# Kernel optimization log

Measured on AMD Instinct MI355X. Metric: run time of the kernel, lower is better.

The kernel has to match this reference:

```python
import jax, jax.numpy as jnp
import numpy as np
import math

C_S, C_Z = 384, 128
N_HEAD, C = 12, 16
N_QP, N_PV = 4, 8
B, N_RES = 1, 384


def quat_to_rot(q):
    # q: (..., 4) unnormalized quaternion -> (..., 3, 3) rotation matrix
    q = q / jnp.linalg.norm(q, axis=-1, keepdims=True)
    w, x, y, z = q[..., 0], q[..., 1], q[..., 2], q[..., 3]
    R = jnp.stack([
        1 - 2 * (y * y + z * z), 2 * (x * y - w * z), 2 * (x * z + w * y),
        2 * (x * y + w * z), 1 - 2 * (x * x + z * z), 2 * (y * z - w * x),
        2 * (x * z - w * y), 2 * (y * z + w * x), 1 - 2 * (x * x + y * y),
    ], axis=-1)
    return R.reshape(q.shape[:-1] + (3, 3))


def warp_3d_point(T, p):
    # T: (..., 1, 1, N, 4, 4) rigid transforms; p: (..., H, P, N, 3)
    R = T[..., :3, :3]
    t = T[..., :3, 3]
    return jnp.squeeze(R @ p[..., None], -1) + t


def warp_3d_point_inv(T, p):
    # Inverse rigid transform: R^T (p - t)
    R = T[..., :3, :3]
    t = T[..., :3, 3]
    return jnp.squeeze(jnp.swapaxes(R, -1, -2) @ (p - t)[..., None], -1)


def setup_inputs() -> dict:
    key = jax.random.key(0)
    ks = jax.random.split(key, 24)
    s = jax.random.normal(ks[0], (B, N_RES, C_S), dtype=jnp.float32)
    z = jax.random.normal(ks[1], (B, N_RES, N_RES, C_Z), dtype=jnp.float32)
    # Build rigid backbone transforms T (rotation from random quaternion + translation)
    quat = jax.random.normal(ks[2], (B, N_RES, 4), dtype=jnp.float32)
    trans = jax.random.normal(ks[3], (B, N_RES, 3), dtype=jnp.float32) * 10.0
    R = quat_to_rot(quat)
    T = jnp.zeros((B, N_RES, 4, 4), dtype=jnp.float32)
    T = T.at[..., :3, :3].set(R)
    T = T.at[..., :3, 3].set(trans)
    T = T.at[..., 3, 3].set(1.0)

    def lin(k, din, dout):
        kw, kb = jax.random.split(k)
        W = jax.random.normal(kw, (din, dout), dtype=jnp.float32) * 0.02
        b = jax.random.normal(kb, (dout,), dtype=jnp.float32) * 0.01
        return W, b

    Wq, bq = lin(ks[4], C_S, N_HEAD * C)
    Wk, bk = lin(ks[5], C_S, N_HEAD * C)
    Wv, bv = lin(ks[6], C_S, N_HEAD * C)
    Wqp, bqp = lin(ks[7], C_S, 3 * N_QP * N_HEAD)
    Wkp, bkp = lin(ks[8], C_S, 3 * N_QP * N_HEAD)
    Wvp, bvp = lin(ks[9], C_S, 3 * N_PV * N_HEAD)
    Wb, bb = lin(ks[10], C_Z, N_HEAD)
    d_out_in = N_HEAD * C_Z + N_HEAD * C + N_HEAD * 4 * N_PV
    Wo, bo = lin(ks[11], d_out_in, C_S)
    head_weights = jax.random.normal(ks[12], (N_HEAD,), dtype=jnp.float32) * 0.1
    return dict(s=s, z=z, T=T, Wq=Wq, bq=bq, Wk=Wk, bk=bk, Wv=Wv, bv=bv,
                Wqp=Wqp, bqp=bqp, Wkp=Wkp, bkp=bkp, Wvp=Wvp, bvp=bvp,
                Wb=Wb, bb=bb, Wo=Wo, bo=bo, head_weights=head_weights)


def ipa_forward(s, z, T, Wq, bq, Wk, bk, Wv, bv, Wqp, bqp, Wkp, bkp,
                Wvp, bvp, Wb, bb, Wo, bo, head_weights):
    batch = s.shape[:-2]
    n = s.shape[-2]
    # --- prepare qkv ---
    def heads(x):  # (..., N, H*C) -> (..., H, N, C)
        return jnp.moveaxis(x.reshape(batch + (n, N_HEAD, C)), -3, -2)
    q = heads(s @ Wq + bq)
    k = heads(s @ Wk + bk)
    v = heads(s @ Wv + bv)

    def pts(x, P):  # (..., N, 3*H*P) -> (..., H, P, N, 3)
        x = x.reshape(batch + (n, 3, N_HEAD, P))
        return jnp.moveaxis(x, (-4, -3), (-2, -1))
    qp = pts(s @ Wqp + bqp, N_QP)
    kp = pts(s @ Wkp + bkp, N_QP)
    vp = pts(s @ Wvp + bvp, N_PV)

    # --- attention scores (Alg 22 line 7) ---
    wc = math.sqrt(2.0 / (9.0 * N_QP))
    wl = math.sqrt(1.0 / 3.0)
    gamma = jax.nn.softplus(head_weights).reshape(-1, 1, 1)  # (H,1,1)
    q = q * (1.0 / math.sqrt(C))
    bias = jnp.moveaxis(z @ Wb + bb, -1, -3)  # (..., H, N, N)
    qk = jnp.einsum('...hic,...hjc->...hij', q, k)
    T_bc = T.reshape(batch + (1, 1, n, 4, 4))
    tqp = warp_3d_point(T_bc, qp)[..., :, None, :]   # (..., H, QP, N, 1, 3)
    tkp = warp_3d_point(T_bc, kp)[..., None, :, :]   # (..., H, QP, 1, N, 3)
    sq_dist = jnp.sum((tqp - tkp) ** 2, axis=-1)      # (..., H, QP, N, N)
    qpkp_term = gamma * (wc / 2.0) * jnp.sum(sq_dist, axis=-3)  # (..., H, N, N)
    att = jax.nn.softmax(wl * (qk + bias - qpkp_term), axis=-1)

    # --- outputs ---
    pairwise = jnp.einsum('...ijc,...hij->...hic', z, att)
    pairwise = jnp.moveaxis(pairwise, -3, -2).reshape(batch + (n, N_HEAD * C_Z))
    v_out = jnp.einsum('...hij,...hjc->...hic', att, v)
    v_out = jnp.moveaxis(v_out, -3, -2).reshape(batch + (n, N_HEAD * C))
    vt = warp_3d_point(T_bc, vp)                                # (..., H, PV, N, 3)
    v_att = jnp.einsum('...hij,...hkjp->...hkip', att, vt)     # (..., H, PV, N, 3)
    v_tr = warp_3d_point_inv(T_bc, v_att)                       # (..., H, PV, N, 3)
    v_tr = jnp.einsum('...hpic->...ichp', v_tr)                 # (..., N, 3, H, PV)
    norm = jnp.linalg.norm(v_tr, axis=-3, keepdims=True)        # (..., N, 1, H, PV)
    vp_norm = norm.reshape(batch + (n, N_HEAD * N_PV))
    vp_out = v_tr.reshape(batch + (n, 3 * N_HEAD * N_PV))

    out = jnp.concatenate([v_out, vp_out, vp_norm, pairwise], axis=-1)
    return out @ Wo + bo


def reference(s, z, T, Wq, bq, Wk, bk, Wv, bv, Wqp, bqp, Wkp, bkp,
              Wvp, bvp, Wb, bb, Wo, bo, head_weights):
    return ipa_forward(s, z, T, Wq, bq, Wk, bk, Wv, bv, Wqp, bqp, Wkp, bkp,
                       Wvp, bvp, Wb, bb, Wo, bo, head_weights)
```

## Files before the change

kernel.cpp:

```cpp
#include <hip/hip_runtime.h>
#include <math.h>

#define NRES 384
#define NH   12
#define WLc 0.5773502691896258f
#define WCc 0.23570226039551587f

typedef __attribute__((ext_vector_type(8))) short short8;
typedef __attribute__((ext_vector_type(4))) float f32x4;

#define OFF_P    0
#define OFF_BIASB 0
#define OFF_QE   884736
#define OFF_KE   1032192
#define OFF_VET  1179648
#define OFF_O40  1290240
#define OFF_SBF  1474560
#define OFF_WCT  1548288
#define OFF_BCT  1769472
#define OFF_WOT  1770624
#define OFF_CAT  2176128
#define OFF_ATT  2581632

__device__ inline unsigned short f2bf(float f) {
    union { float f; unsigned u; } v; v.f = f;
    unsigned u = v.u;
    return (unsigned short)((u + 0x7FFFu + ((u >> 16) & 1u)) >> 16);
}
__device__ inline float bf2f(unsigned short h) {
    union { unsigned u; float f; } v; v.u = ((unsigned)h) << 16;
    return v.f;
}

__global__ __launch_bounds__(256) void pack_kernel(
    const float* __restrict__ s,
    const float* __restrict__ Wq,  const float* __restrict__ bq,
    const float* __restrict__ Wk,  const float* __restrict__ bk,
    const float* __restrict__ Wv,  const float* __restrict__ bv,
    const float* __restrict__ Wqp, const float* __restrict__ bqp,
    const float* __restrict__ Wkp, const float* __restrict__ bkp,
    const float* __restrict__ Wvp, const float* __restrict__ bvp,
    const float* __restrict__ Wo,
    float* __restrict__ ws)
{
    int id = blockIdx.x * 256 + threadIdx.x;
    unsigned short* sbf  = (unsigned short*)(ws + OFF_SBF);
    unsigned short* wct  = (unsigned short*)(ws + OFF_WCT);
    unsigned short* wot  = (unsigned short*)(ws + OFF_WOT);
    float* bct = ws + OFF_BCT;

    if (id < 36864) {
        const float4 v = ((const float4*)s)[id];
        unsigned short r[4] = { f2bf(v.x), f2bf(v.y), f2bf(v.z), f2bf(v.w) };
        *(uint2*)(sbf + id * 4) = *(uint2*)r;
        return;
    }
    id -= 36864;
    if (id < 55296) {
        int n = id / 48, k8 = (id % 48) * 8;
        const float* W; int dout, col;
        if      (n < 192) { W = Wq;  dout = 192; col = n; }
        else if (n < 384) { W = Wk;  dout = 192; col = n - 192; }
        else if (n < 576) { W = Wv;  dout = 192; col = n - 384; }
        else if (n < 720) { W = Wqp; dout = 144; col = n - 576; }
        else if (n < 864) { W = Wkp; dout = 144; col = n - 720; }
        else              { W = Wvp; dout = 288; col = n - 864; }
        unsigned short r[8];
        #pragma unroll
        for (int j = 0; j < 8; j++) r[j] = f2bf(W[(size_t)(k8 + j) * dout + col]);
        *(uint4*)(wct + (size_t)n * 384 + k8) = *(uint4*)r;
        return;
    }
    id -= 55296;
    if (id < 101376) {
        int n = id / 264, k8 = (id % 264) * 8;
        unsigned short r[8];
        #pragma unroll
        for (int j = 0; j < 8; j++) r[j] = f2bf(Wo[(size_t)(k8 + j) * 384 + n]);
        *(uint4*)(wot + (size_t)n * 2112 + k8) = *(uint4*)r;
        return;
    }
    id -= 101376;
    if (id < 1152) {
        int n = id; float b;
        if      (n < 192) b = bq[n];
        else if (n < 384) b = bk[n - 192];
        else if (n < 576) b = bv[n - 384];
        else if (n < 720) b = bqp[n - 576];
        else if (n < 864) b = bkp[n - 720];
        else              b = bvp[n - 864];
        bct[n] = b;
    }
}

__global__ __launch_bounds__(256) void proj_mfma(float* __restrict__ ws)
{
    const unsigned short* sbf = (const unsigned short*)(ws + OFF_SBF);
    const unsigned short* wct = (const unsigned short*)(ws + OFF_WCT);
    const float* bct = ws + OFF_BCT;
    float* P = ws + OFF_P;

    int t = threadIdx.x, w = t >> 6, lane = t & 63;
    int m = lane & 15, q = lane >> 4;
    int n0 = blockIdx.x * 64, m0 = blockIdx.y * 64 + w * 16;

    f32x4 acc[4] = {0};
    const unsigned short* arow = sbf + (size_t)(m0 + m) * 384;
    #pragma unroll 4
    for (int s = 0; s < 12; s++) {
        int k = s * 32 + q * 8;
        short8 a = *(const short8*)(arow + k);
        #pragma unroll
        for (int nt = 0; nt < 4; nt++) {
            short8 b = *(const short8*)(wct + (size_t)(n0 + nt * 16 + m) * 384 + k);
            acc[nt] = __builtin_amdgcn_mfma_f32_16x16x32_bf16(a, b, acc[nt], 0, 0, 0);
        }
    }
    #pragma unroll
    for (int nt = 0; nt < 4; nt++) {
        int col = n0 + nt * 16 + m;
        float bias = bct[col];
        #pragma unroll
        for (int r = 0; r < 4; r++) {
            int row = m0 + q * 4 + r;
            P[(size_t)row * 1152 + col] = acc[nt][r] + bias;
        }
    }
}

__global__ __launch_bounds__(256) void prep_kernel(
    const float* __restrict__ T, const float* __restrict__ hw,
    float* __restrict__ ws)
{
    int id = blockIdx.x * 256 + threadIdx.x;
    if (id >= NH * NRES) return;
    int h = id / NRES, i = id % NRES;
    const float* P = ws + OFF_P;
    const float* pr = P + (size_t)i * 1152;

    float R[3][3], tr[3];
    #pragma unroll
    for (int r = 0; r < 3; r++) {
        #pragma unroll
        for (int c = 0; c < 3; c++) R[r][c] = T[i * 16 + r * 4 + c];
        tr[r] = T[i * 16 + r * 4 + 3];
    }
    float x = hw[h];
    float g = (x > 20.f) ? x : log1pf(expf(x));

    float* Qe = ws + OFF_QE + (size_t)(h * NRES + i) * 32;
    float* Ke = ws + OFF_KE + (size_t)(h * NRES + i) * 32;
    #pragma unroll
    for (int c = 0; c < 16; c++) {
        Qe[c] = WLc * 0.25f * pr[h * 16 + c];
        Ke[c] = pr[192 + h * 16 + c];
    }
    float sqq = 0.f, sqk = 0.f;
    float gw = WLc * g * WCc;
    #pragma unroll
    for (int p = 0; p < 4; p++) {
        float a0 = pr[576 + 0 * 48 + h * 4 + p];
        float a1 = pr[576 + 1 * 48 + h * 4 + p];
        float a2 = pr[576 + 2 * 48 + h * 4 + p];
        float b0 = pr[720 + 0 * 48 + h * 4 + p];
        float b1 = pr[720 + 1 * 48 + h * 4 + p];
        float b2 = pr[720 + 2 * 48 + h * 4 + p];
        #pragma unroll
        for (int r = 0; r < 3; r++) {
            float tq = R[r][0] * a0 + R[r][1] * a1 + R[r][2] * a2 + tr[r];
            float tk = R[r][0] * b0 + R[r][1] * b1 + R[r][2] * b2 + tr[r];
            Qe[16 + p * 3 + r] = gw * tq;
            Ke[16 + p * 3 + r] = tk;
            sqq += tq * tq;  sqk += tk * tk;
        }
    }
    Qe[28] = -0.5f * gw;  Qe[29] = -0.5f * gw * sqq;  Qe[30] = 0.f; Qe[31] = 0.f;
    Ke[28] = sqk;         Ke[29] = 1.f;               Ke[30] = 0.f; Ke[31] = 0.f;

    unsigned short* vet = (unsigned short*)(ws + OFF_VET);
    #pragma unroll
    for (int c = 0; c < 16; c++)
        vet[(size_t)(h * 48 + c) * 384 + i] = f2bf(pr[384 + h * 16 + c]);
    #pragma unroll
    for (int p = 0; p < 8; p++) {
        float a0 = pr[864 + 0 * 96 + h * 8 + p];
        float a1 = pr[864 + 1 * 96 + h * 8 + p];
        float a2 = pr[864 + 2 * 96 + h * 8 + p];
        #pragma unroll
        for (int r = 0; r < 3; r++)
            vet[(size_t)(h * 48 + 16 + p * 3 + r) * 384 + i] =
                f2bf(R[r][0] * a0 + R[r][1] * a1 + R[r][2] * a2 + tr[r]);
    }
    #pragma unroll
    for (int c = 40; c < 48; c++) vet[(size_t)(h * 48 + c) * 384 + i] = 0;
}

__global__ __launch_bounds__(256) void bias_mfma(
    const float* __restrict__ z, const float* __restrict__ Wb,
    const float* __restrict__ bb, float* __restrict__ ws)
{
    __shared__ unsigned short zb[64 * 136];
    __shared__ unsigned short wbT[16 * 136];
    __shared__ float sbb[16];
    unsigned short* biasb = (unsigned short*)(ws + OFF_BIASB);

    int t = threadIdx.x;
    size_t m0 = (size_t)blockIdx.x * 64;

    {
        int r = t >> 2, co = (t & 3) * 32;
        const float* zr = z + (m0 + r) * 128 + co;
        #pragma unroll
        for (int u = 0; u < 4; u++) {
            float4 v0 = ((const float4*)zr)[u * 2 + 0];
            float4 v1 = ((const float4*)zr)[u * 2 + 1];
            unsigned short rr[8] = { f2bf(v0.x), f2bf(v0.y), f2bf(v0.z), f2bf(v0.w),
                                     f2bf(v1.x), f2bf(v1.y), f2bf(v1.z), f2bf(v1.w) };
            *(uint4*)(zb + r * 136 + co + u * 8) = *(uint4*)rr;
        }
    }
    if (t < 128) {
        #pragma unroll
        for (int h = 0; h < 12; h++) wbT[h * 136 + t] = f2bf(Wb[t * 12 + h]);
        #pragma unroll
        for (int h = 12; h < 16; h++) wbT[h * 136 + t] = 0;
    }
    if (t < 16) sbb[t] = (t < 12) ? bb[t] : 0.f;
    __syncthreads();

    int w = t >> 6, lane = t & 63;
    int m = lane & 15, q = lane >> 4;
    f32x4 acc = {0};
    #pragma unroll
    for (int s = 0; s < 4; s++) {
        int k = s * 32 + q * 8;
        short8 a = *(const short8*)(zb + (w * 16 + m) * 136 + k);
        short8 b = *(const short8*)(wbT + m * 136 + k);
        acc = __builtin_amdgcn_mfma_f32_16x16x32_bf16(a, b, acc, 0, 0, 0);
    }
    int h = m;
    if (h < 12) {
        #pragma unroll
        for (int r = 0; r < 4; r++) {
            size_t ri = m0 + w * 16 + q * 4 + r;
            biasb[(size_t)h * 147456 + ri] = f2bf(WLc * (acc[r] + sbb[h]));
        }
    }
}

__global__ __launch_bounds__(512) void logits_kernel(float* __restrict__ ws)
{
    __shared__ float sQe[8 * 32];
    __shared__ float sLg[8][384];
    __shared__ float sMS[16];

    int h = blockIdx.y, i0 = blockIdx.x * 8;
    int t = threadIdx.x;
    const float* Qe = ws + OFF_QE;
    const float* Ke = ws + OFF_KE;
    const unsigned short* biasb = (const unsigned short*)(ws + OFF_BIASB);
    unsigned short* attb = (unsigned short*)(ws + OFF_ATT);

    if (t < 256)
        sQe[t] = Qe[(size_t)(h * 384 + i0 + (t >> 5)) * 32 + (t & 31)];
    __syncthreads();

    float lgv[8];
    if (t < 384) {
        int j = t;
        float ke[32];
        const float4* kr = (const float4*)(Ke + (size_t)(h * 384 + j) * 32);
        #pragma unroll
        for (int u = 0; u < 8; u++) { float4 v = kr[u]; ke[u*4]=v.x; ke[u*4+1]=v.y; ke[u*4+2]=v.z; ke[u*4+3]=v.w; }
        #pragma unroll
        for (int ii = 0; ii < 8; ii++) {
            float acc = 0.f;
            #pragma unroll
            for (int c = 0; c < 32; c++) acc += sQe[ii * 32 + c] * ke[c];
            acc += bf2f(biasb[(size_t)(h * 384 + i0 + ii) * 384 + j]);
            lgv[ii] = acc;
            sLg[ii][j] = acc;
        }
    }
    __syncthreads();
    {
        int w = t >> 6, lane = t & 63;
        float vv[6], mx = -1e30f;
        #pragma unroll
        for (int u = 0; u < 6; u++) { vv[u] = sLg[w][lane + 64 * u]; mx = fmaxf(mx, vv[u]); }
        #pragma unroll
        for (int off = 1; off < 64; off <<= 1) mx = fmaxf(mx, __shfl_xor(mx, off));
        float sm = 0.f;
        #pragma unroll
        for (int u = 0; u < 6; u++) sm += __expf(vv[u] - mx);
        #pragma unroll
        for (int off = 1; off < 64; off <<= 1) sm += __shfl_xor(sm, off);
        if (lane == 0) { sMS[w] = mx; sMS[8 + w] = sm; }
    }
    __syncthreads();
    if (t < 384) {
        int j = t;
        #pragma unroll
        for (int ii = 0; ii < 8; ii++) {
            float a = __expf(lgv[ii] - sMS[ii]) * (1.0f / sMS[8 + ii]);
            attb[(size_t)(h * 384 + i0 + ii) * 384 + j] = f2bf(a);
        }
    }
}

__global__ __launch_bounds__(128) void out40_mfma(float* __restrict__ ws)
{
    const unsigned short* attb = (const unsigned short*)(ws + OFF_ATT);
    const unsigned short* vet  = (const unsigned short*)(ws + OFF_VET);
    float* o40 = ws + OFF_O40;

    int h = blockIdx.y;
    int t = threadIdx.x, w = t >> 6, lane = t & 63;
    int m = lane & 15, q = lane >> 4;
    int m0 = blockIdx.x * 32 + w * 16;

    f32x4 acc[3] = {0};
    const unsigned short* arow = attb + (size_t)(h * 384 + m0 + m) * 384;
    #pragma unroll 3
    for (int s = 0; s < 12; s++) {
        int k = s * 32 + q * 8;
        short8 a = *(const short8*)(arow + k);
        #pragma unroll
        for (int nt = 0; nt < 3; nt++) {
            short8 b = *(const short8*)(vet + (size_t)(h * 48 + nt * 16 + m) * 384 + k);
            acc[nt] = __builtin_amdgcn_mfma_f32_16x16x32_bf16(a, b, acc[nt], 0, 0, 0);
        }
    }
    #pragma unroll
    for (int nt = 0; nt < 3; nt++) {
        int c = nt * 16 + m;
        if (c < 40) {
            #pragma unroll
            for (int r = 0; r < 4; r++) {
                int row = m0 + q * 4 + r;
                o40[(size_t)row * 480 + h * 40 + c] = acc[nt][r];
            }
        }
    }
}

__global__ __launch_bounds__(256) void pairwise_pts(
    const float* __restrict__ z, const float* __restrict__ T,
    float* __restrict__ ws)
{
    __shared__ unsigned short zt[128 * 40];
    __shared__ float sT16[16];

    int i = blockIdx.x;
    int t = threadIdx.x, w = t >> 6, lane = t & 63;
    int m = lane & 15, q = lane >> 4;
    const unsigned short* attb = (const unsigned short*)(ws + OFF_ATT);
    unsigned short* catb = (unsigned short*)(ws + OFF_CAT) ;
    const float* o40 = ws + OFF_O40;

    if (t < 16) sT16[t] = T[i * 16 + t];

    f32x4 acc0 = {0}, acc1 = {0};
    int cst = t & 63, jg = t >> 6;
    for (int kt = 0; kt < 12; kt++) {
        int j0 = kt * 32;
        __syncthreads();
        {
            int j8 = j0 + jg * 8;
            const float* zb = z + ((size_t)i * 384 + j8) * 128 + cst;
            unsigned short r0[8], r1[8];
            #pragma unroll
            for (int jj = 0; jj < 8; jj++) {
                r0[jj] = f2bf(zb[(size_t)jj * 128]);
                r1[jj] = f2bf(zb[(size_t)jj * 128 + 64]);
            }
            *(uint4*)(zt + cst * 40 + jg * 8)        = *(uint4*)r0;
            *(uint4*)(zt + (cst + 64) * 40 + jg * 8) = *(uint4*)r1;
        }
        __syncthreads();
        short8 a;
        if (m < 12) a = *(const short8*)(attb + ((size_t)(m * 384 + i)) * 384 + j0 + q * 8);
        else        a = (short8){0,0,0,0,0,0,0,0};
        short8 b0 = *(const short8*)(zt + (w * 32 + m) * 40 + q * 8);
        short8 b1 = *(const short8*)(zt + (w * 32 + 16 + m) * 40 + q * 8);
        acc0 = __builtin_amdgcn_mfma_f32_16x16x32_bf16(a, b0, acc0, 0, 0, 0);
        acc1 = __builtin_amdgcn_mfma_f32_16x16x32_bf16(a, b1, acc1, 0, 0, 0);
    }
    {
        unsigned short* crow = catb + (size_t)i * 2112 + 576;
        #pragma unroll
        for (int r = 0; r < 4; r++) {
            int h = q * 4 + r;
            if (h < 12) {
                crow[h * 128 + w * 32 + m]      = f2bf(acc0[r]);
                crow[h * 128 + w * 32 + 16 + m] = f2bf(acc1[r]);
            }
        }
    }
    __syncthreads();
    if (t < 192)
        catb[(size_t)i * 2112 + t] = f2bf(o40[(size_t)i * 480 + (t >> 4) * 40 + (t & 15)]);
    if (t < 96) {
        int h = t >> 3, p = t & 7;
        const float* o = o40 + (size_t)i * 480 + h * 40 + 16 + p * 3;
        float x0 = o[0] - sT16[3];
        float x1 = o[1] - sT16[7];
        float x2 = o[2] - sT16[11];
        float r0 = sT16[0] * x0 + sT16[4] * x1 + sT16[8]  * x2;
        float r1 = sT16[1] * x0 + sT16[5] * x1 + sT16[9]  * x2;
        float r2 = sT16[2] * x0 + sT16[6] * x1 + sT16[10] * x2;
        unsigned short* crow = catb + (size_t)i * 2112;
        crow[192 + 0 * 96 + h * 8 + p] = f2bf(r0);
        crow[192 + 1 * 96 + h * 8 + p] = f2bf(r1);
        crow[192 + 2 * 96 + h * 8 + p] = f2bf(r2);
        crow[480 + h * 8 + p] = f2bf(sqrtf(r0 * r0 + r1 * r1 + r2 * r2));
    }
}

__global__ __launch_bounds__(256) void out_init(const float* __restrict__ bo, float* __restrict__ out)
{
    int idx = blockIdx.x * 256 + threadIdx.x;
    if (idx < 384 * 384) out[idx] = bo[idx % 384];
}

__global__ __launch_bounds__(256) void outgemm_mfma(float* __restrict__ ws, float* __restrict__ out)
{
    const unsigned short* catb = (const unsigned short*)(ws + OFF_CAT);
    const unsigned short* wot  = (const unsigned short*)(ws + OFF_WOT);

    int t = threadIdx.x, w = t >> 6, lane = t & 63;
    int m = lane & 15, q = lane >> 4;
    int n0 = blockIdx.x * 64, m0 = blockIdx.y * 64 + w * 16;
    int kbase = blockIdx.z * 704;

    f32x4 acc[4] = {0};
    const unsigned short* arow = catb + (size_t)(m0 + m) * 2112;
    #pragma unroll 2
    for (int s = 0; s < 22; s++) {
        int k = kbase + s * 32 + q * 8;
        short8 a = *(const short8*)(arow + k);
        #pragma unroll
        for (int nt = 0; nt < 4; nt++) {
            short8 b = *(const short8*)(wot + (size_t)(n0 + nt * 16 + m) * 2112 + k);
            acc[nt] = __builtin_amdgcn_mfma_f32_16x16x32_bf16(a, b, acc[nt], 0, 0, 0);
        }
    }
    #pragma unroll
    for (int nt = 0; nt < 4; nt++) {
        int col = n0 + nt * 16 + m;
        #pragma unroll
        for (int r = 0; r < 4; r++) {
            int row = m0 + q * 4 + r;
            atomicAdd(&out[(size_t)row * 384 + col], acc[nt][r]);
        }
    }
}

extern "C" void kernel_launch(void* const* d_in, const int* in_sizes, int n_in,
                              void* d_out, int out_size, void* d_ws, size_t ws_size,
                              hipStream_t stream)
{
    const float* s   = (const float*)d_in[0];
    const float* z   = (const float*)d_in[1];
    const float* T   = (const float*)d_in[2];
    const float* Wq  = (const float*)d_in[3];
    const float* bq  = (const float*)d_in[4];
    const float* Wk  = (const float*)d_in[5];
    const float* bk  = (const float*)d_in[6];
    const float* Wv  = (const float*)d_in[7];
    const float* bv  = (const float*)d_in[8];
    const float* Wqp = (const float*)d_in[9];
    const float* bqp = (const float*)d_in[10];
    const float* Wkp = (const float*)d_in[11];
    const float* bkp = (const float*)d_in[12];
    const float* Wvp = (const float*)d_in[13];
    const float* bvp = (const float*)d_in[14];
    const float* Wb  = (const float*)d_in[15];
    const float* bb  = (const float*)d_in[16];
    const float* Wo  = (const float*)d_in[17];
    const float* bo  = (const float*)d_in[18];
    const float* hw  = (const float*)d_in[19];
    float* ws  = (float*)d_ws;
    float* out = (float*)d_out;

    pack_kernel<<<(36864 + 55296 + 101376 + 1152 + 255) / 256, 256, 0, stream>>>(
        s, Wq, bq, Wk, bk, Wv, bv, Wqp, bqp, Wkp, bkp, Wvp, bvp, Wo, ws);
    proj_mfma<<<dim3(18, 6), 256, 0, stream>>>(ws);
    prep_kernel<<<18, 256, 0, stream>>>(T, hw, ws);
    bias_mfma<<<2304, 256, 0, stream>>>(z, Wb, bb, ws);
    logits_kernel<<<dim3(48, 12), 512, 0, stream>>>(ws);
    out40_mfma<<<dim3(12, 12), 128, 0, stream>>>(ws);
    pairwise_pts<<<384, 256, 0, stream>>>(z, T, ws);
    out_init<<<576, 256, 0, stream>>>(bo, out);
    outgemm_mfma<<<dim3(6, 6, 3), 256, 0, stream>>>(ws, out);
}
```

Baseline: 241.0 us.

## Fuse pair bias, softmax and attention outputs into one flash-style kernel

Replaces the separate bias, logits, softmax, value-output and pairwise kernels with a single per-residue flash kernel. It reads z once per row chunk, computes the pair bias, runs an online softmax, and accumulates value, point and pairwise outputs without writing the full bias and attention matrices to memory. The code also switches from bf16 to fp16 MFMA and parallelises prep across residues. In exchange, only 384 blocks do serial chunk loops and the online rescaling adds some work.

```diff
diff --git a/kernel.cpp b/kernel.cpp
--- a/kernel.cpp
+++ b/kernel.cpp
@@ -6,31 +6,19 @@
 #define WLc 0.5773502691896258f
 #define WCc 0.23570226039551587f
 
-typedef __attribute__((ext_vector_type(8))) short short8;
+typedef __attribute__((ext_vector_type(8))) _Float16 half8;
 typedef __attribute__((ext_vector_type(4))) float f32x4;
 
 #define OFF_P    0
-#define OFF_BIASB 0
-#define OFF_QE   884736
-#define OFF_KE   1032192
-#define OFF_VET  1179648
-#define OFF_O40  1290240
-#define OFF_SBF  1474560
-#define OFF_WCT  1548288
-#define OFF_BCT  1769472
-#define OFF_WOT  1770624
-#define OFF_CAT  2176128
-#define OFF_ATT  2581632
-
-__device__ inline unsigned short f2bf(float f) {
-    union { float f; unsigned u; } v; v.f = f;
-    unsigned u = v.u;
-    return (unsigned short)((u + 0x7FFFu + ((u >> 16) & 1u)) >> 16);
-}
-__device__ inline float bf2f(unsigned short h) {
-    union { unsigned u; float f; } v; v.u = ((unsigned)h) << 16;
-    return v.f;
-}
+#define OFF_QE   442368
+#define OFF_KE   589824
+#define OFF_VET  737280
+#define OFF_SH   847872
+#define OFF_WCT  921600
+#define OFF_BCT  1142784
+#define OFF_WOT  1143936
+#define OFF_WBT  1549440
+#define OFF_CAT  1550464
 
 __global__ __launch_bounds__(256) void pack_kernel(
     const float* __restrict__ s,
@@ -40,19 +28,20 @@
     const float* __restrict__ Wqp, const float* __restrict__ bqp,
     const float* __restrict__ Wkp, const float* __restrict__ bkp,
     const float* __restrict__ Wvp, const float* __restrict__ bvp,
-    const float* __restrict__ Wo,
+    const float* __restrict__ Wb,  const float* __restrict__ Wo,
     float* __restrict__ ws)
 {
     int id = blockIdx.x * 256 + threadIdx.x;
-    unsigned short* sbf  = (unsigned short*)(ws + OFF_SBF);
-    unsigned short* wct  = (unsigned short*)(ws + OFF_WCT);
-    unsigned short* wot  = (unsigned short*)(ws + OFF_WOT);
+    _Float16* sh  = (_Float16*)(ws + OFF_SH);
+    _Float16* wct = (_Float16*)(ws + OFF_WCT);
+    _Float16* wot = (_Float16*)(ws + OFF_WOT);
+    _Float16* wbt = (_Float16*)(ws + OFF_WBT);
     float* bct = ws + OFF_BCT;
 
     if (id < 36864) {
         const float4 v = ((const float4*)s)[id];
-        unsigned short r[4] = { f2bf(v.x), f2bf(v.y), f2bf(v.z), f2bf(v.w) };
-        *(uint2*)(sbf + id * 4) = *(uint2*)r;
+        _Float16 r[4] = { (_Float16)v.x, (_Float16)v.y, (_Float16)v.z, (_Float16)v.w };
+        *(uint2*)(sh + id * 4) = *(uint2*)r;
         return;
     }
     id -= 36864;
@@ -65,22 +54,28 @@
         else if (n < 720) { W = Wqp; dout = 144; col = n - 576; }
         else if (n < 864) { W = Wkp; dout = 144; col = n - 720; }
         else              { W = Wvp; dout = 288; col = n - 864; }
-        unsigned short r[8];
-        #pragma unroll
-        for (int j = 0; j < 8; j++) r[j] = f2bf(W[(size_t)(k8 + j) * dout + col]);
-        *(uint4*)(wct + (size_t)n * 384 + k8) = *(uint4*)r;
+        half8 r;
+        #pragma unroll
+        for (int j = 0; j < 8; j++) r[j] = (_Float16)W[(size_t)(k8 + j) * dout + col];
+        *(half8*)(wct + (size_t)n * 384 + k8) = r;
         return;
     }
     id -= 55296;
     if (id < 101376) {
         int n = id / 264, k8 = (id % 264) * 8;
-        unsigned short r[8];
-        #pragma unroll
-        for (int j = 0; j < 8; j++) r[j] = f2bf(Wo[(size_t)(k8 + j) * 384 + n]);
-        *(uint4*)(wot + (size_t)n * 2112 + k8) = *(uint4*)r;
+        half8 r;
+        #pragma unroll
+        for (int j = 0; j < 8; j++) r[j] = (_Float16)Wo[(size_t)(k8 + j) * 384 + n];
+        *(half8*)(wot + (size_t)n * 2112 + k8) = r;
         return;
     }
     id -= 101376;
+    if (id < 2048) {
+        int h = id >> 7, c = id & 127;
+        wbt[h * 128 + c] = (h < 12) ? (_Float16)(WLc * Wb[c * 12 + h]) : (_Float16)0.f;
+        return;
+    }
+    id -= 2048;
     if (id < 1152) {
         int n = id; float b;
         if      (n < 192) b = bq[n];
@@ -95,8 +90,8 @@
 
 __global__ __launch_bounds__(256) void proj_mfma(float* __restrict__ ws)
 {
-    const unsigned short* sbf = (const unsigned short*)(ws + OFF_SBF);
-    const unsigned short* wct = (const unsigned short*)(ws + OFF_WCT);
+    const _Float16* sh  = (const _Float16*)(ws + OFF_SH);
+    const _Float16* wct = (const _Float16*)(ws + OFF_WCT);
     const float* bct = ws + OFF_BCT;
     float* P = ws + OFF_P;
 
@@ -105,15 +100,15 @@
     int n0 = blockIdx.x * 64, m0 = blockIdx.y * 64 + w * 16;
 
     f32x4 acc[4] = {0};
-    const unsigned short* arow = sbf + (size_t)(m0 + m) * 384;
+    const _Float16* arow = sh + (size_t)(m0 + m) * 384;
     #pragma unroll 4
     for (int s = 0; s < 12; s++) {
         int k = s * 32 + q * 8;
-        short8 a = *(const short8*)(arow + k);
+        half8 a = *(const half8*)(arow + k);
         #pragma unroll
         for (int nt = 0; nt < 4; nt++) {
-            short8 b = *(const short8*)(wct + (size_t)(n0 + nt * 16 + m) * 384 + k);
-            acc[nt] = __builtin_amdgcn_mfma_f32_16x16x32_bf16(a, b, acc[nt], 0, 0, 0);
+            half8 b = *(const half8*)(wct + (size_t)(n0 + nt * 16 + m) * 384 + k);
+            acc[nt] = __builtin_amdgcn_mfma_f32_16x16x32_f16(a, b, acc[nt], 0, 0, 0);
         }
     }
     #pragma unroll
@@ -121,299 +116,256 @@
         int col = n0 + nt * 16 + m;
         float bias = bct[col];
         #pragma unroll
-        for (int r = 0; r < 4; r++) {
-            int row = m0 + q * 4 + r;
-            P[(size_t)row * 1152 + col] = acc[nt][r] + bias;
-        }
-    }
-}
-
-__global__ __launch_bounds__(256) void prep_kernel(
+        for (int r = 0; r < 4; r++)
+            P[(size_t)(m0 + q * 4 + r) * 1152 + col] = acc[nt][r] + bias;
+    }
+}
+
+__global__ __launch_bounds__(192) void prep_kernel(
     const float* __restrict__ T, const float* __restrict__ hw,
     float* __restrict__ ws)
 {
-    int id = blockIdx.x * 256 + threadIdx.x;
-    if (id >= NH * NRES) return;
-    int h = id / NRES, i = id % NRES;
-    const float* P = ws + OFF_P;
-    const float* pr = P + (size_t)i * 1152;
-
-    float R[3][3], tr[3];
-    #pragma unroll
-    for (int r = 0; r < 3; r++) {
-        #pragma unroll
-        for (int c = 0; c < 3; c++) R[r][c] = T[i * 16 + r * 4 + c];
-        tr[r] = T[i * 16 + r * 4 + 3];
-    }
-    float x = hw[h];
-    float g = (x > 20.f) ? x : log1pf(expf(x));
-
-    float* Qe = ws + OFF_QE + (size_t)(h * NRES + i) * 32;
-    float* Ke = ws + OFF_KE + (size_t)(h * NRES + i) * 32;
-    #pragma unroll
-    for (int c = 0; c < 16; c++) {
-        Qe[c] = WLc * 0.25f * pr[h * 16 + c];
-        Ke[c] = pr[192 + h * 16 + c];
-    }
-    float sqq = 0.f, sqk = 0.f;
-    float gw = WLc * g * WCc;
-    #pragma unroll
-    for (int p = 0; p < 4; p++) {
-        float a0 = pr[576 + 0 * 48 + h * 4 + p];
-        float a1 = pr[576 + 1 * 48 + h * 4 + p];
-        float a2 = pr[576 + 2 * 48 + h * 4 + p];
-        float b0 = pr[720 + 0 * 48 + h * 4 + p];
-        float b1 = pr[720 + 1 * 48 + h * 4 + p];
-        float b2 = pr[720 + 2 * 48 + h * 4 + p];
-        #pragma unroll
-        for (int r = 0; r < 3; r++) {
-            float tq = R[r][0] * a0 + R[r][1] * a1 + R[r][2] * a2 + tr[r];
-            float tk = R[r][0] * b0 + R[r][1] * b1 + R[r][2] * b2 + tr[r];
-            Qe[16 + p * 3 + r] = gw * tq;
-            Ke[16 + p * 3 + r] = tk;
-            sqq += tq * tq;  sqk += tk * tk;
-        }
-    }
-    Qe[28] = -0.5f * gw;  Qe[29] = -0.5f * gw * sqq;  Qe[30] = 0.f; Qe[31] = 0.f;
-    Ke[28] = sqk;         Ke[29] = 1.f;               Ke[30] = 0.f; Ke[31] = 0.f;
-
-    unsigned short* vet = (unsigned short*)(ws + OFF_VET);
-    #pragma unroll
-    for (int c = 0; c < 16; c++)
-        vet[(size_t)(h * 48 + c) * 384 + i] = f2bf(pr[384 + h * 16 + c]);
-    #pragma unroll
-    for (int p = 0; p < 8; p++) {
-        float a0 = pr[864 + 0 * 96 + h * 8 + p];
-        float a1 = pr[864 + 1 * 96 + h * 8 + p];
-        float a2 = pr[864 + 2 * 96 + h * 8 + p];
-        #pragma unroll
-        for (int r = 0; r < 3; r++)
-            vet[(size_t)(h * 48 + 16 + p * 3 + r) * 384 + i] =
-                f2bf(R[r][0] * a0 + R[r][1] * a1 + R[r][2] * a2 + tr[r]);
-    }
-    #pragma unroll
-    for (int c = 40; c < 48; c++) vet[(size_t)(h * 48 + c) * 384 + i] = 0;
-}
-
-__global__ __launch_bounds__(256) void bias_mfma(
-    const float* __restrict__ z, const float* __restrict__ Wb,
+    int i = blockIdx.x, t = threadIdx.x;
+    const float* pr = ws + OFF_P + (size_t)i * 1152;
+    float* Qe = ws + OFF_QE;
+    float* Ke = ws + OFF_KE;
+    _Float16* vet = (_Float16*)(ws + OFF_VET);
+
+    __shared__ float sT[16], sG[12];
+    __shared__ float sTQ[12][4][3], sTK[12][4][3];
+    if (t < 16) sT[t] = T[i * 16 + t];
+    if (t < 12) { float x = hw[t]; sG[t] = (x > 20.f) ? x : log1pf(__expf(x)); }
+    __syncthreads();
+    float R00=sT[0],R01=sT[1],R02=sT[2],t0=sT[3];
+    float R10=sT[4],R11=sT[5],R12=sT[6],t1=sT[7];
+    float R20=sT[8],R21=sT[9],R22=sT[10],t2=sT[11];
+
+    if (t < 48) {
+        int h = t >> 2, p = t & 3;
+        float a0 = pr[576 + 0*48 + h*4 + p], a1 = pr[576 + 1*48 + h*4 + p], a2 = pr[576 + 2*48 + h*4 + p];
+        sTQ[h][p][0] = R00*a0 + R01*a1 + R02*a2 + t0;
+        sTQ[h][p][1] = R10*a0 + R11*a1 + R12*a2 + t1;
+        sTQ[h][p][2] = R20*a0 + R21*a1 + R22*a2 + t2;
+    } else if (t < 96) {
+        int tt = t - 48, h = tt >> 2, p = tt & 3;
+        float a0 = pr[720 + 0*48 + h*4 + p], a1 = pr[720 + 1*48 + h*4 + p], a2 = pr[720 + 2*48 + h*4 + p];
+        sTK[h][p][0] = R00*a0 + R01*a1 + R02*a2 + t0;
+        sTK[h][p][1] = R10*a0 + R11*a1 + R12*a2 + t1;
+        sTK[h][p][2] = R20*a0 + R21*a1 + R22*a2 + t2;
+    } else {
+        int tt = t - 96, h = tt >> 3, p = tt & 7;
+        float a0 = pr[864 + 0*96 + h*8 + p], a1 = pr[864 + 1*96 + h*8 + p], a2 = pr[864 + 2*96 + h*8 + p];
+        vet[(size_t)(h*48 + 16 + p*3 + 0) * 384 + i] = (_Float16)(R00*a0 + R01*a1 + R02*a2 + t0);
+        vet[(size_t)(h*48 + 16 + p*3 + 1) * 384 + i] = (_Float16)(R10*a0 + R11*a1 + R12*a2 + t1);
+        vet[(size_t)(h*48 + 16 + p*3 + 2) * 384 + i] = (_Float16)(R20*a0 + R21*a1 + R22*a2 + t2);
+    }
+    {
+        int h = t >> 4, c = t & 15;
+        vet[(size_t)(h*48 + c) * 384 + i] = (_Float16)pr[384 + h*16 + c];
+        if (t < 96) vet[(size_t)((t>>3)*48 + 40 + (t&7)) * 384 + i] = (_Float16)0.f;
+    }
+    {
+        int h = t >> 4, c = t & 15;
+        Qe[(size_t)i*384 + h*32 + c] = WLc * 0.25f * pr[h*16 + c];
+        Ke[((size_t)h*384 + i)*32 + c] = pr[192 + h*16 + c];
+    }
+    __syncthreads();
+    if (t < 144) {
+        int h = t / 12, d = t % 12, p = d / 3, r = d % 3;
+        float gw = WLc * sG[h] * WCc;
+        Qe[(size_t)i*384 + h*32 + 16 + d] = gw * sTQ[h][p][r];
+        Ke[((size_t)h*384 + i)*32 + 16 + d] = sTK[h][p][r];
+    }
+    if (t < 12) {
+        int h = t;
+        float sqq = 0.f, sqk = 0.f;
+        #pragma unroll
+        for (int p = 0; p < 4; p++)
+            #pragma unroll
+            for (int r = 0; r < 3; r++) { sqq += sTQ[h][p][r]*sTQ[h][p][r]; sqk += sTK[h][p][r]*sTK[h][p][r]; }
+        float gw = WLc * sG[h] * WCc;
+        Qe[(size_t)i*384 + h*32 + 28] = -0.5f * gw;
+        Qe[(size_t)i*384 + h*32 + 29] = -0.5f * gw * sqq;
+        Qe[(size_t)i*384 + h*32 + 30] = 0.f;
+        Qe[(size_t)i*384 + h*32 + 31] = 0.f;
+        Ke[((size_t)h*384 + i)*32 + 28] = sqk;
+        Ke[((size_t)h*384 + i)*32 + 29] = 1.f;
+        Ke[((size_t)h*384 + i)*32 + 30] = 0.f;
+        Ke[((size_t)h*384 + i)*32 + 31] = 0.f;
+    }
+}
+
+__global__ __launch_bounds__(256) void flash_kernel(
+    const float* __restrict__ z, const float* __restrict__ T,
     const float* __restrict__ bb, float* __restrict__ ws)
 {
-    __shared__ unsigned short zb[64 * 136];
-    __shared__ unsigned short wbT[16 * 136];
-    __shared__ float sbb[16];
-    unsigned short* biasb = (unsigned short*)(ws + OFF_BIASB);
-
-    int t = threadIdx.x;
-    size_t m0 = (size_t)blockIdx.x * 64;
-
-    {
-        int r = t >> 2, co = (t & 3) * 32;
-        const float* zr = z + (m0 + r) * 128 + co;
-        #pragma unroll
-        for (int u = 0; u < 4; u++) {
-            float4 v0 = ((const float4*)zr)[u * 2 + 0];
-            float4 v1 = ((const float4*)zr)[u * 2 + 1];
-            unsigned short rr[8] = { f2bf(v0.x), f2bf(v0.y), f2bf(v0.z), f2bf(v0.w),
-                                     f2bf(v1.x), f2bf(v1.y), f2bf(v1.z), f2bf(v1.w) };
-            *(uint4*)(zb + r * 136 + co + u * 8) = *(uint4*)rr;
-        }
-    }
-    if (t < 128) {
-        #pragma unroll
-        for (int h = 0; h < 12; h++) wbT[h * 136 + t] = f2bf(Wb[t * 12 + h]);
-        #pragma unroll
-        for (int h = 12; h < 16; h++) wbT[h * 136 + t] = 0;
-    }
-    if (t < 16) sbb[t] = (t < 12) ? bb[t] : 0.f;
-    __syncthreads();
-
-    int w = t >> 6, lane = t & 63;
-    int m = lane & 15, q = lane >> 4;
-    f32x4 acc = {0};
-    #pragma unroll
-    for (int s = 0; s < 4; s++) {
-        int k = s * 32 + q * 8;
-        short8 a = *(const short8*)(zb + (w * 16 + m) * 136 + k);
-        short8 b = *(const short8*)(wbT + m * 136 + k);
-        acc = __builtin_amdgcn_mfma_f32_16x16x32_bf16(a, b, acc, 0, 0, 0);
-    }
-    int h = m;
-    if (h < 12) {
-        #pragma unroll
-        for (int r = 0; r < 4; r++) {
-            size_t ri = m0 + w * 16 + q * 4 + r;
-            biasb[(size_t)h * 147456 + ri] = f2bf(WLc * (acc[r] + sbb[h]));
-        }
-    }
-}
-
-__global__ __launch_bounds__(512) void logits_kernel(float* __restrict__ ws)
-{
-    __shared__ float sQe[8 * 32];
-    __shared__ float sLg[8][384];
-    __shared__ float sMS[16];
-
-    int h = blockIdx.y, i0 = blockIdx.x * 8;
-    int t = threadIdx.x;
+    int i = blockIdx.x, t = threadIdx.x, w = t >> 6, lane = t & 63;
+    int m16 = lane & 15, q = lane >> 4;
+
+    __shared__ _Float16 zc[64 * 136];
+    __shared__ _Float16 attc[16 * 72];
+    __shared__ _Float16 wbl[16 * 136];
+    __shared__ float bias_ch[64 * 17];
+    __shared__ float sQe[384];
+    __shared__ float sT[16], sBB[12], sM[12], sL[12], sAl[16], sInv[12];
+    __shared__ float sO[480];
+
     const float* Qe = ws + OFF_QE;
     const float* Ke = ws + OFF_KE;
-    const unsigned short* biasb = (const unsigned short*)(ws + OFF_BIASB);
-    unsigned short* attb = (unsigned short*)(ws + OFF_ATT);
-
-    if (t < 256)
-        sQe[t] = Qe[(size_t)(h * 384 + i0 + (t >> 5)) * 32 + (t & 31)];
-    __syncthreads();
-
-    float lgv[8];
-    if (t < 384) {
-        int j = t;
-        float ke[32];
-        const float4* kr = (const float4*)(Ke + (size_t)(h * 384 + j) * 32);
-        #pragma unroll
-        for (int u = 0; u < 8; u++) { float4 v = kr[u]; ke[u*4]=v.x; ke[u*4+1]=v.y; ke[u*4+2]=v.z; ke[u*4+3]=v.w; }
-        #pragma unroll
-        for (int ii = 0; ii < 8; ii++) {
-            float acc = 0.f;
-            #pragma unroll
-            for (int c = 0; c < 32; c++) acc += sQe[ii * 32 + c] * ke[c];
-            acc += bf2f(biasb[(size_t)(h * 384 + i0 + ii) * 384 + j]);
-            lgv[ii] = acc;
-            sLg[ii][j] = acc;
-        }
-    }
-    __syncthreads();
+    const _Float16* vet = (const _Float16*)(ws + OFF_VET);
+    const _Float16* wbt = (const _Float16*)(ws + OFF_WBT);
+    _Float16* crow = (_Float16*)(ws + OFF_CAT) + (size_t)i * 2112;
+
+    if (t < 16) sT[t] = T[i * 16 + t];
+    if (t < 12) { sBB[t] = WLc * bb[t]; sM[t] = -1e30f; sL[t] = 0.f; }
+    if (t >= 12 && t < 16) sAl[t] = 0.f;
+    for (int e = t; e < 384; e += 256) sQe[e] = Qe[(size_t)i * 384 + e];
     {
-        int w = t >> 6, lane = t & 63;
-        float vv[6], mx = -1e30f;
-        #pragma unroll
-        for (int u = 0; u < 6; u++) { vv[u] = sLg[w][lane + 64 * u]; mx = fmaxf(mx, vv[u]); }
-        #pragma unroll
-        for (int off = 1; off < 64; off <<= 1) mx = fmaxf(mx, __shfl_xor(mx, off));
-        float sm = 0.f;
-        #pragma unroll
-        for (int u = 0; u < 6; u++) sm += __expf(vv[u] - mx);
-        #pragma unroll
-        for (int off = 1; off < 64; off <<= 1) sm += __shfl_xor(sm, off);
-        if (lane == 0) { sMS[w] = mx; sMS[8 + w] = sm; }
-    }
-    __syncthreads();
-    if (t < 384) {
-        int j = t;
-        #pragma unroll
-        for (int ii = 0; ii < 8; ii++) {
-            float a = __expf(lgv[ii] - sMS[ii]) * (1.0f / sMS[8 + ii]);
-            attb[(size_t)(h * 384 + i0 + ii) * 384 + j] = f2bf(a);
-        }
-    }
-}
-
-__global__ __launch_bounds__(128) void out40_mfma(float* __restrict__ ws)
-{
-    const unsigned short* attb = (const unsigned short*)(ws + OFF_ATT);
-    const unsigned short* vet  = (const unsigned short*)(ws + OFF_VET);
-    float* o40 = ws + OFF_O40;
-
-    int h = blockIdx.y;
-    int t = threadIdx.x, w = t >> 6, lane = t & 63;
-    int m = lane & 15, q = lane >> 4;
-    int m0 = blockIdx.x * 32 + w * 16;
-
-    f32x4 acc[3] = {0};
-    const unsigned short* arow = attb + (size_t)(h * 384 + m0 + m) * 384;
-    #pragma unroll 3
-    for (int s = 0; s < 12; s++) {
-        int k = s * 32 + q * 8;
-        short8 a = *(const short8*)(arow + k);
-        #pragma unroll
-        for (int nt = 0; nt < 3; nt++) {
-            short8 b = *(const short8*)(vet + (size_t)(h * 48 + nt * 16 + m) * 384 + k);
-            acc[nt] = __builtin_amdgcn_mfma_f32_16x16x32_bf16(a, b, acc[nt], 0, 0, 0);
-        }
-    }
-    #pragma unroll
-    for (int nt = 0; nt < 3; nt++) {
-        int c = nt * 16 + m;
-        if (c < 40) {
-            #pragma unroll
-            for (int r = 0; r < 4; r++) {
-                int row = m0 + q * 4 + r;
-                o40[(size_t)row * 480 + h * 40 + c] = acc[nt][r];
-            }
-        }
-    }
-}
-
-__global__ __launch_bounds__(256) void pairwise_pts(
-    const float* __restrict__ z, const float* __restrict__ T,
-    float* __restrict__ ws)
-{
-    __shared__ unsigned short zt[128 * 40];
-    __shared__ float sT16[16];
-
-    int i = blockIdx.x;
-    int t = threadIdx.x, w = t >> 6, lane = t & 63;
-    int m = lane & 15, q = lane >> 4;
-    const unsigned short* attb = (const unsigned short*)(ws + OFF_ATT);
-    unsigned short* catb = (unsigned short*)(ws + OFF_CAT) ;
-    const float* o40 = ws + OFF_O40;
-
-    if (t < 16) sT16[t] = T[i * 16 + t];
-
-    f32x4 acc0 = {0}, acc1 = {0};
-    int cst = t & 63, jg = t >> 6;
-    for (int kt = 0; kt < 12; kt++) {
-        int j0 = kt * 32;
+        int row = t >> 4, c8 = (t & 15) * 8;
+        *(half8*)(wbl + row * 136 + c8) = *(const half8*)(wbt + row * 128 + c8);
+    }
+    for (int e = t; e < 4 * 72; e += 256) attc[12 * 72 + e] = (_Float16)0.f;
+    __syncthreads();
+
+    f32x4 apw[2] = {0};
+    float ao0 = 0.f, ao1 = 0.f;
+    int h40 = t / 20, c40 = (t % 20) * 2;
+
+    for (int ch = 0; ch < 6; ch++) {
+        int j0 = ch * 64;
         __syncthreads();
         {
-            int j8 = j0 + jg * 8;
-            const float* zb = z + ((size_t)i * 384 + j8) * 128 + cst;
-            unsigned short r0[8], r1[8];
-            #pragma unroll
-            for (int jj = 0; jj < 8; jj++) {
-                r0[jj] = f2bf(zb[(size_t)jj * 128]);
-                r1[jj] = f2bf(zb[(size_t)jj * 128 + 64]);
-            }
-            *(uint4*)(zt + cst * 40 + jg * 8)        = *(uint4*)r0;
-            *(uint4*)(zt + (cst + 64) * 40 + jg * 8) = *(uint4*)r1;
+            int jr = t >> 2, cg = (t & 3) * 32;
+            const float* zp = z + ((size_t)i * 384 + j0 + jr) * 128 + cg;
+            #pragma unroll
+            for (int u = 0; u < 4; u++) {
+                float4 v0 = ((const float4*)zp)[u * 2];
+                float4 v1 = ((const float4*)zp)[u * 2 + 1];
+                half8 r;
+                r[0]=(_Float16)v0.x; r[1]=(_Float16)v0.y; r[2]=(_Float16)v0.z; r[3]=(_Float16)v0.w;
+                r[4]=(_Float16)v1.x; r[5]=(_Float16)v1.y; r[6]=(_Float16)v1.z; r[7]=(_Float16)v1.w;
+                *(half8*)(zc + jr * 136 + cg + u * 8) = r;
+            }
         }
         __syncthreads();
-        short8 a;
-        if (m < 12) a = *(const short8*)(attb + ((size_t)(m * 384 + i)) * 384 + j0 + q * 8);
-        else        a = (short8){0,0,0,0,0,0,0,0};
-        short8 b0 = *(const short8*)(zt + (w * 32 + m) * 40 + q * 8);
-        short8 b1 = *(const short8*)(zt + (w * 32 + 16 + m) * 40 + q * 8);
-        acc0 = __builtin_amdgcn_mfma_f32_16x16x32_bf16(a, b0, acc0, 0, 0, 0);
-        acc1 = __builtin_amdgcn_mfma_f32_16x16x32_bf16(a, b1, acc1, 0, 0, 0);
-    }
+        {
+            f32x4 bacc = {0};
+            #pragma unroll
+            for (int s = 0; s < 4; s++) {
+                half8 a = *(const half8*)(zc + (w * 16 + m16) * 136 + s * 32 + q * 8);
+                half8 b = *(const half8*)(wbl + m16 * 136 + s * 32 + q * 8);
+                bacc = __builtin_amdgcn_mfma_f32_16x16x32_f16(a, b, bacc, 0, 0, 0);
+            }
+            #pragma unroll
+            for (int r = 0; r < 4; r++)
+                bias_ch[(w * 16 + q * 4 + r) * 17 + m16] = bacc[r];
+        }
+        __syncthreads();
+        {
+            #pragma unroll
+            for (int u = 0; u < 3; u++) {
+                int h = w * 3 + u;
+                float lg = bias_ch[lane * 17 + h] + sBB[h];
+                const float4* k4 = (const float4*)(Ke + ((size_t)h * 384 + j0 + lane) * 32);
+                #pragma unroll
+                for (int uu = 0; uu < 8; uu++) {
+                    float4 kv = k4[uu];
+                    lg += sQe[h*32 + uu*4 + 0] * kv.x + sQe[h*32 + uu*4 + 1] * kv.y
+                        + sQe[h*32 + uu*4 + 2] * kv.z + sQe[h*32 + uu*4 + 3] * kv.w;
+                }
+                float mx = lg;
+                #pragma unroll
+                for (int off = 1; off < 64; off <<= 1) mx = fmaxf(mx, __shfl_xor(mx, off));
+                float mold = sM[h];
+                float mnew = fmaxf(mold, mx);
+                float e = __expf(lg - mnew);
+                float ssum = e;
+                #pragma unroll
+                for (int off = 1; off < 64; off <<= 1) ssum += __shfl_xor(ssum, off);
+                float alpha = __expf(mold - mnew);
+                if (lane == 0) { sM[h] = mnew; sL[h] = sL[h] * alpha + ssum; sAl[h] = alpha; }
+                attc[h * 72 + lane] = (_Float16)e;
+            }
+        }
+        __syncthreads();
+        {
+            float al[4];
+            #pragma unroll
+            for (int r = 0; r < 4; r++) al[r] = sAl[q * 4 + r];
+            #pragma unroll
+            for (int sub = 0; sub < 2; sub++)
+                #pragma unroll
+                for (int r = 0; r < 4; r++) apw[sub][r] *= al[r];
+            #pragma unroll
+            for (int ks = 0; ks < 2; ks++) {
+                half8 a = *(const half8*)(attc + m16 * 72 + ks * 32 + q * 8);
+                #pragma unroll
+                for (int sub = 0; sub < 2; sub++) {
+                    int c = w * 32 + sub * 16 + m16;
+                    half8 b;
+                    #pragma unroll
+                    for (int jj = 0; jj < 8; jj++) b[jj] = zc[(ks * 32 + q * 8 + jj) * 136 + c];
+                    apw[sub] = __builtin_amdgcn_mfma_f32_16x16x32_f16(a, b, apw[sub], 0, 0, 0);
+                }
+            }
+        }
+        if (t < 240) {
+            float al = sAl[h40];
+            float a0 = ao0 * al, a1 = ao1 * al;
+            const _Float16* vp0 = vet + ((size_t)(h40 * 48 + c40)) * 384 + j0;
+            const _Float16* vp1 = vp0 + 384;
+            #pragma unroll
+            for (int hf = 0; hf < 2; hf++) {
+                half8 v0[4], v1[4];
+                #pragma unroll
+                for (int u = 0; u < 4; u++) {
+                    v0[u] = *(const half8*)(vp0 + hf * 32 + u * 8);
+                    v1[u] = *(const half8*)(vp1 + hf * 32 + u * 8);
+                }
+                #pragma unroll
+                for (int u = 0; u < 4; u++)
+                    #pragma unroll
+                    for (int jj = 0; jj < 8; jj++) {
+                        float av = (float)attc[h40 * 72 + hf * 32 + u * 8 + jj];
+                        a0 += av * (float)v0[u][jj];
+                        a1 += av * (float)v1[u][jj];
+                    }
+            }
+            ao0 = a0; ao1 = a1;
+        }
+    }
+    __syncthreads();
+    if (t < 12) sInv[t] = 1.0f / sL[t];
+    __syncthreads();
     {
-        unsigned short* crow = catb + (size_t)i * 2112 + 576;
-        #pragma unroll
-        for (int r = 0; r < 4; r++) {
-            int h = q * 4 + r;
-            if (h < 12) {
-                crow[h * 128 + w * 32 + m]      = f2bf(acc0[r]);
-                crow[h * 128 + w * 32 + 16 + m] = f2bf(acc1[r]);
-            }
-        }
-    }
-    __syncthreads();
-    if (t < 192)
-        catb[(size_t)i * 2112 + t] = f2bf(o40[(size_t)i * 480 + (t >> 4) * 40 + (t & 15)]);
+        #pragma unroll
+        for (int sub = 0; sub < 2; sub++)
+            #pragma unroll
+            for (int r = 0; r < 4; r++) {
+                int h = q * 4 + r;
+                if (h < 12)
+                    crow[576 + h * 128 + w * 32 + sub * 16 + m16] = (_Float16)(apw[sub][r] * sInv[h]);
+            }
+    }
+    if (t < 240) {
+        sO[h40 * 40 + c40]     = ao0 * sInv[h40];
+        sO[h40 * 40 + c40 + 1] = ao1 * sInv[h40];
+    }
+    __syncthreads();
+    if (t < 192) crow[t] = (_Float16)sO[(t >> 4) * 40 + (t & 15)];
     if (t < 96) {
         int h = t >> 3, p = t & 7;
-        const float* o = o40 + (size_t)i * 480 + h * 40 + 16 + p * 3;
-        float x0 = o[0] - sT16[3];
-        float x1 = o[1] - sT16[7];
-        float x2 = o[2] - sT16[11];
-        float r0 = sT16[0] * x0 + sT16[4] * x1 + sT16[8]  * x2;
-        float r1 = sT16[1] * x0 + sT16[5] * x1 + sT16[9]  * x2;
-        float r2 = sT16[2] * x0 + sT16[6] * x1 + sT16[10] * x2;
-        unsigned short* crow = catb + (size_t)i * 2112;
-        crow[192 + 0 * 96 + h * 8 + p] = f2bf(r0);
-        crow[192 + 1 * 96 + h * 8 + p] = f2bf(r1);
-        crow[192 + 2 * 96 + h * 8 + p] = f2bf(r2);
-        crow[480 + h * 8 + p] = f2bf(sqrtf(r0 * r0 + r1 * r1 + r2 * r2));
+        const float* o = sO + h * 40 + 16 + p * 3;
+        float x0 = o[0] - sT[3];
+        float x1 = o[1] - sT[7];
+        float x2 = o[2] - sT[11];
+        float r0 = sT[0]*x0 + sT[4]*x1 + sT[8]*x2;
+        float r1 = sT[1]*x0 + sT[5]*x1 + sT[9]*x2;
+        float r2 = sT[2]*x0 + sT[6]*x1 + sT[10]*x2;
+        crow[192 + 0*96 + h*8 + p] = (_Float16)r0;
+        crow[192 + 1*96 + h*8 + p] = (_Float16)r1;
+        crow[192 + 2*96 + h*8 + p] = (_Float16)r2;
+        crow[480 + h*8 + p] = (_Float16)sqrtf(r0*r0 + r1*r1 + r2*r2);
     }
 }
 
@@ -425,8 +377,8 @@
 
 __global__ __launch_bounds__(256) void outgemm_mfma(float* __restrict__ ws, float* __restrict__ out)
 {
-    const unsigned short* catb = (const unsigned short*)(ws + OFF_CAT);
-    const unsigned short* wot  = (const unsigned short*)(ws + OFF_WOT);
+    const _Float16* catb = (const _Float16*)(ws + OFF_CAT);
+    const _Float16* wot  = (const _Float16*)(ws + OFF_WOT);
 
     int t = threadIdx.x, w = t >> 6, lane = t & 63;
     int m = lane & 15, q = lane >> 4;
@@ -434,25 +386,23 @@
     int kbase = blockIdx.z * 704;
 
     f32x4 acc[4] = {0};
-    const unsigned short* arow = catb + (size_t)(m0 + m) * 2112;
+    const _Float16* arow = catb + (size_t)(m0 + m) * 2112;
     #pragma unroll 2
     for (int s = 0; s < 22; s++) {
         int k = kbase + s * 32 + q * 8;
-        short8 a = *(const short8*)(arow + k);
+        half8 a = *(const half8*)(arow + k);
         #pragma unroll
         for (int nt = 0; nt < 4; nt++) {
-            short8 b = *(const short8*)(wot + (size_t)(n0 + nt * 16 + m) * 2112 + k);
-            acc[nt] = __builtin_amdgcn_mfma_f32_16x16x32_bf16(a, b, acc[nt], 0, 0, 0);
+            half8 b = *(const half8*)(wot + (size_t)(n0 + nt * 16 + m) * 2112 + k);
+            acc[nt] = __builtin_amdgcn_mfma_f32_16x16x32_f16(a, b, acc[nt], 0, 0, 0);
         }
     }
     #pragma unroll
     for (int nt = 0; nt < 4; nt++) {
         int col = n0 + nt * 16 + m;
         #pragma unroll
-        for (int r = 0; r < 4; r++) {
-            int row = m0 + q * 4 + r;
-            atomicAdd(&out[(size_t)row * 384 + col], acc[nt][r]);
-        }
+        for (int r = 0; r < 4; r++)
+            atomicAdd(&out[(size_t)(m0 + q * 4 + r) * 384 + col], acc[nt][r]);
     }
 }
 
@@ -483,14 +433,11 @@
     float* ws  = (float*)d_ws;
     float* out = (float*)d_out;
 
-    pack_kernel<<<(36864 + 55296 + 101376 + 1152 + 255) / 256, 256, 0, stream>>>(
-        s, Wq, bq, Wk, bk, Wv, bv, Wqp, bqp, Wkp, bkp, Wvp, bvp, Wo, ws);
+    pack_kernel<<<769, 256, 0, stream>>>(s, Wq, bq, Wk, bk, Wv, bv,
+                                         Wqp, bqp, Wkp, bkp, Wvp, bvp, Wb, Wo, ws);
     proj_mfma<<<dim3(18, 6), 256, 0, stream>>>(ws);
-    prep_kernel<<<18, 256, 0, stream>>>(T, hw, ws);
-    bias_mfma<<<2304, 256, 0, stream>>>(z, Wb, bb, ws);
-    logits_kernel<<<dim3(48, 12), 512, 0, stream>>>(ws);
-    out40_mfma<<<dim3(12, 12), 128, 0, stream>>>(ws);
-    pairwise_pts<<<384, 256, 0, stream>>>(z, T, ws);
+    prep_kernel<<<384, 192, 0, stream>>>(T, hw, ws);
+    flash_kernel<<<384, 256, 0, stream>>>(z, T, bb, ws);
     out_init<<<576, 256, 0, stream>>>(bo, out);
     outgemm_mfma<<<dim3(6, 6, 3), 256, 0, stream>>>(ws, out);
 }
```

After: 252.4 us. 4.7% more time.
